# Kernel optimization log

Hardware: AMD Instinct MI355X
Metric: run time of the kernel (lower is better)

Reference implementation:

```python
import jax, jax.numpy as jnp
import numpy as np

DIM = 192
HEADS = 6
HEAD_DIM = DIM // HEADS
WS = (7, 7, 7)
SHIFT = (3, 3, 3)
RES = (14, 56, 56)
MLP_HIDDEN = DIM * 4
N = WS[0] * WS[1] * WS[2]  # 343 tokens per window
SCALE = HEAD_DIM ** (-0.5)


def _rel_pos_index():
    coords = np.stack(np.meshgrid(np.arange(WS[0]), np.arange(WS[1]), np.arange(WS[2]), indexing='ij'))
    cf = coords.reshape(3, -1)  # (3, N)
    rel = (cf[:, :, None] - cf[:, None, :]).transpose(1, 2, 0).astype(np.int64)  # (N, N, 3)
    rel[..., 0] += WS[0] - 1
    rel[..., 1] += WS[1] - 1
    rel[..., 2] += WS[2] - 1
    rel[..., 0] *= (2 * WS[1] - 1) * (2 * WS[2] - 1)
    rel[..., 1] *= 2 * WS[2] - 1
    return rel.sum(-1)  # (N, N)


def _attn_mask():
    S, H, W = RES
    img = np.zeros((S, H, W), dtype=np.float32)
    cnt = 0
    for s in (slice(0, -WS[0]), slice(-WS[0], -SHIFT[0]), slice(-SHIFT[0], None)):
        for h in (slice(0, -WS[1]), slice(-WS[1], -SHIFT[1]), slice(-SHIFT[1], None)):
            for w in (slice(0, -WS[2]), slice(-WS[2], -SHIFT[2]), slice(-SHIFT[2], None)):
                img[s, h, w] = cnt
                cnt += 1
    m = img.reshape(S // WS[0], WS[0], H // WS[1], WS[1], W // WS[2], WS[2])
    m = m.transpose(0, 2, 4, 1, 3, 5).reshape(-1, N)  # (nW, N)
    diff = m[:, None, :] - m[:, :, None]
    return np.where(diff != 0, -100.0, 0.0).astype(np.float32)  # (nW, N, N)


REL_IDX = jnp.asarray(_rel_pos_index())
ATTN_MASK = jnp.asarray(_attn_mask())


def _window_partition(x):
    # x: (B, S, H, W, C) -> (B*nW, N, C)
    B, S, H, W, C = x.shape
    x = x.reshape(B, S // WS[0], WS[0], H // WS[1], WS[1], W // WS[2], WS[2], C)
    x = x.transpose(0, 1, 3, 5, 2, 4, 6, 7)
    return x.reshape(-1, N, C)


def _window_reverse(wins, B):
    S, H, W = RES
    C = wins.shape[-1]
    x = wins.reshape(B, S // WS[0], H // WS[1], W // WS[2], WS[0], WS[1], WS[2], C)
    x = x.transpose(0, 1, 4, 2, 5, 3, 6, 7)
    return x.reshape(B, S, H, W, C)


def _layernorm(x, g, b):
    mu = x.mean(-1, keepdims=True)
    var = ((x - mu) ** 2).mean(-1, keepdims=True)
    return (x - mu) * jax.lax.rsqrt(var + 1e-5) * g + b


def setup_inputs() -> dict:
    key = jax.random.key(0)
    ks = jax.random.split(key, 16)
    p = lambda k, shape, s=0.02: (jax.random.normal(k, shape, dtype=jnp.float32) * s)
    return {
        'x': jax.random.normal(ks[0], (1, DIM) + RES, dtype=jnp.float32),
        'norm1_g': jnp.ones((DIM,), jnp.float32),
        'norm1_b': jnp.zeros((DIM,), jnp.float32),
        'qkv_w': p(ks[1], (DIM, 3 * DIM)),
        'qkv_b': jnp.zeros((3 * DIM,), jnp.float32),
        'rpb_table': p(ks[2], ((2 * WS[0] - 1) * (2 * WS[1] - 1) * (2 * WS[2] - 1), HEADS)),
        'proj_w': p(ks[3], (DIM, DIM)),
        'proj_b': jnp.zeros((DIM,), jnp.float32),
        'norm2_g': jnp.ones((DIM,), jnp.float32),
        'norm2_b': jnp.zeros((DIM,), jnp.float32),
        'fc1_w': p(ks[4], (DIM, MLP_HIDDEN)),
        'fc1_b': jnp.zeros((MLP_HIDDEN,), jnp.float32),
        'fc2_w': p(ks[5], (MLP_HIDDEN, DIM)),
        'fc2_b': jnp.zeros((DIM,), jnp.float32),
    }


def reference(x, norm1_g, norm1_b, qkv_w, qkv_b, rpb_table, proj_w, proj_b,
              norm2_g, norm2_b, fc1_w, fc1_b, fc2_w, fc2_b):
    B, C, S, H, W = x.shape
    L = S * H * W
    xt = x.transpose(0, 2, 3, 4, 1).reshape(B, L, C)  # b (s h w) c
    shortcut = xt
    xn = _layernorm(xt, norm1_g, norm1_b).reshape(B, S, H, W, C)
    xs = jnp.roll(xn, (-SHIFT[0], -SHIFT[1], -SHIFT[2]), axis=(1, 2, 3))
    xw = _window_partition(xs)  # (B*nW, N, C)
    B_ = xw.shape[0]
    nW = B_ // B

    qkv = (xw @ qkv_w + qkv_b).reshape(B_, N, 3, HEADS, HEAD_DIM)
    q = qkv[:, :, 0].transpose(0, 2, 1, 3) * SCALE  # (B_, h, N, d)
    k = qkv[:, :, 1].transpose(0, 2, 1, 3)
    v = qkv[:, :, 2].transpose(0, 2, 1, 3)

    attn = jnp.einsum('bhnd,bhmd->bhnm', q, k)
    bias = rpb_table[REL_IDX.reshape(-1)].reshape(N, N, HEADS).transpose(2, 0, 1)  # (h, N, N)
    attn = attn + bias[None]
    attn = attn.reshape(B, nW, HEADS, N, N) + ATTN_MASK[None, :, None]
    attn = jax.nn.softmax(attn.reshape(B_, HEADS, N, N), axis=-1)

    out = jnp.einsum('bhnm,bhmd->bhnd', attn, v).transpose(0, 2, 1, 3).reshape(B_, N, C)
    out = out @ proj_w + proj_b

    xr = _window_reverse(out, B)
    xr = jnp.roll(xr, (SHIFT[0], SHIFT[1], SHIFT[2]), axis=(1, 2, 3)).reshape(B, L, C)
    xt = shortcut + xr

    h = _layernorm(xt, norm2_g, norm2_b)
    h = jax.nn.gelu(h @ fc1_w + fc1_b, approximate=False) @ fc2_w + fc2_b
    xt = xt + h

    return xt.reshape(B, S, H, W, C).transpose(0, 4, 1, 2, 3)  # (B, C, S, H, W)
```

## Files before the change

kernel.cpp:

```cpp
#include <hip/hip_runtime.h>
#include <hip/hip_bf16.h>
#include <math.h>

#define L_TOK 43904
#define NWIN 128
#define NTOK 343
#define NHEAD 6
#define SCALE 0.17677669529663687f
#define LOG2E 1.4426950408889634f
#define NMASK -144.26950408889634f
#define BSTRIDE 352

typedef __attribute__((ext_vector_type(8))) short short8;
typedef __attribute__((ext_vector_type(4))) float f32x4;

__device__ __forceinline__ unsigned short f2bf(float x) {
    union { float f; unsigned int u; } v; v.f = x;
    unsigned int r = v.u + 0x7fffu + ((v.u >> 16) & 1u);
    return (unsigned short)(r >> 16);
}
__device__ __forceinline__ unsigned int pk2(float a, float b) {
    return (unsigned int)f2bf(a) | ((unsigned int)f2bf(b) << 16);
}
__device__ __forceinline__ void gload16(const void* g, void* l) {
    __builtin_amdgcn_global_load_lds((const __attribute__((address_space(1))) void*)g,
                                     (__attribute__((address_space(3))) void*)l, 16, 0, 0);
}

__device__ __forceinline__ int winrow(int l) {
    int s = l / 3136;
    int rem = l - s * 3136;
    int h = rem / 56;
    int w = rem - h * 56;
    int ps = s + 11; if (ps >= 14) ps -= 14;
    int ph = h + 53; if (ph >= 56) ph -= 56;
    int pw = w + 53; if (pw >= 56) pw -= 56;
    int wi = ((ps / 7) * 8 + ph / 7) * 8 + pw / 7;
    int tk = ((ps % 7) * 7 + ph % 7) * 7 + pw % 7;
    return wi * NTOK + tk;
}

__global__ __launch_bounds__(256) void convert_weights(
    const float* __restrict__ qkv_w, const float* __restrict__ qkv_b,
    const float* __restrict__ proj_w, const float* __restrict__ fc1_w,
    const float* __restrict__ fc2_w,
    unsigned short* __restrict__ qkvT, unsigned short* __restrict__ projT,
    unsigned short* __restrict__ fc1T, unsigned short* __restrict__ fc2T,
    float* __restrict__ qkvb_s) {
    int stride = gridDim.x * 256;
    int t0 = blockIdx.x * 256 + threadIdx.x;
    const float qs = SCALE * LOG2E;
    for (int i = t0; i < 576 * 192; i += stride) {
        int n = i / 192, k = i - n * 192;
        float v = qkv_w[k * 576 + n];
        if (n < 192) v *= qs;
        qkvT[i] = f2bf(v);
    }
    for (int i = t0; i < 192 * 192; i += stride) {
        int n = i / 192, k = i - n * 192;
        projT[i] = f2bf(proj_w[k * 192 + n]);
    }
    for (int i = t0; i < 768 * 192; i += stride) {
        int n = i / 192, k = i - n * 192;
        fc1T[i] = f2bf(fc1_w[k * 768 + n]);
    }
    for (int i = t0; i < 192 * 768; i += stride) {
        int n = i / 768, k = i - n * 768;
        fc2T[i] = f2bf(fc2_w[k * 192 + n]);
    }
    for (int i = t0; i < 576; i += stride) {
        float v = qkv_b[i]; if (i < 192) v *= qs;
        qkvb_s[i] = v;
    }
}

__global__ __launch_bounds__(256) void bias_compact(const float* __restrict__ table, float* __restrict__ biasC) {
    int q = blockIdx.x;
    int qs = q / 49, qh = (q / 7) % 7, qw = q % 7;
    for (int k = threadIdx.x; k < BSTRIDE; k += 256) {
        if (k < NTOK) {
            int ks = k / 49, kh = (k / 7) % 7, kw = k % 7;
            int idx = ((qs - ks + 6) * 13 + (qh - kh + 6)) * 13 + (qw - kw + 6);
            #pragma unroll
            for (int h = 0; h < NHEAD; ++h)
                biasC[((size_t)h * NTOK + q) * BSTRIDE + k] = table[idx * 6 + h] * LOG2E;
        } else {
            #pragma unroll
            for (int h = 0; h < NHEAD; ++h)
                biasC[((size_t)h * NTOK + q) * BSTRIDE + k] = -30000.f;
        }
    }
}

__global__ __launch_bounds__(256) void ln1_part(const float* __restrict__ x,
                                                const float* __restrict__ g, const float* __restrict__ b,
                                                float* __restrict__ xt, unsigned short* __restrict__ xw) {
    __shared__ float tile[192 * 65];
    __shared__ float red[4][64];
    __shared__ float red2[4][64];
    __shared__ float mu_s[64], rs_s[64];
    int l0 = blockIdx.x * 64;
    int tid = threadIdx.x;
    int j = tid & 63, c4 = tid >> 6;
    for (int cb = 0; cb < 192; cb += 4)
        tile[(cb + c4) * 65 + j] = x[(size_t)(cb + c4) * L_TOK + l0 + j];
    __syncthreads();
    float s = 0.f, ss = 0.f;
    for (int c = c4 * 48; c < c4 * 48 + 48; ++c) {
        float v = tile[c * 65 + j];
        s += v; ss += v * v;
    }
    red[c4][j] = s; red2[c4][j] = ss;
    __syncthreads();
    if (tid < 64) {
        float S = red[0][j] + red[1][j] + red[2][j] + red[3][j];
        float SS = red2[0][j] + red2[1][j] + red2[2][j] + red2[3][j];
        float mu = S * (1.f / 192.f);
        float var = SS * (1.f / 192.f) - mu * mu;
        mu_s[j] = mu;
        rs_s[j] = rsqrtf(var + 1e-5f);
    }
    __syncthreads();
    int wave = tid >> 6, lid = tid & 63;
    for (int t = wave; t < 64; t += 4) {
        int l = l0 + t;
        int r = winrow(l);
        float mu = mu_s[t], rs = rs_s[t];
        #pragma unroll
        for (int q = 0; q < 3; ++q) {
            int c = q * 64 + lid;
            float v = tile[c * 65 + t];
            xt[(size_t)l * 192 + c] = v;
            xw[(size_t)r * 192 + c] = f2bf((v - mu) * rs * g[c] + b[c]);
        }
    }
}

template<int EPI, int OUTMODE>
__global__ __launch_bounds__(256, 3) void gemm_bf16(
    const unsigned short* __restrict__ A, const unsigned short* __restrict__ Bt,
    const float* __restrict__ bias, void* __restrict__ Cout,
    const float* __restrict__ xt, int N, int K) {
    __shared__ unsigned char smem[49152];
    unsigned short* sh = (unsigned short*)smem;
    const int tid = threadIdx.x;
    const int m0 = blockIdx.x * 128;
    const int n0 = blockIdx.y * 64;
    const int lane = tid & 63, wv = tid >> 6;
    const int wm = wv >> 1, wn = wv & 1;
    const int lr = lane & 15, lg = lane >> 4;
    const int KT = K >> 6;

    f32x4 acc[4][2];
    #pragma unroll
    for (int i = 0; i < 4; ++i)
        #pragma unroll
        for (int jj = 0; jj < 2; ++jj)
            acc[i][jj] = (f32x4){0.f, 0.f, 0.f, 0.f};

    #define STAGE(BUF, K0) { \
        unsigned short* dst = sh + (BUF) * 12288; \
        _Pragma("unroll") \
        for (int i_ = 0; i_ < 4; ++i_) { \
            int g_ = (i_ * 4 + wv) * 64 + lane; \
            int row_ = g_ >> 3, gc_ = g_ & 7; \
            gload16(A + (size_t)(m0 + row_) * K + (K0) + ((gc_ ^ (row_ & 7)) << 3), dst + g_ * 8); \
        } \
        _Pragma("unroll") \
        for (int i_ = 0; i_ < 2; ++i_) { \
            int g_ = (i_ * 4 + wv) * 64 + lane; \
            int row_ = g_ >> 3, gc_ = g_ & 7; \
            gload16(Bt + (size_t)(n0 + row_) * K + (K0) + ((gc_ ^ (row_ & 7)) << 3), dst + 8192 + g_ * 8); \
        } }

    STAGE(0, 0);
    __syncthreads();
    for (int kt = 0; kt < KT; ++kt) {
        int buf = kt & 1;
        if (kt + 1 < KT) STAGE(buf ^ 1, (kt + 1) << 6);
        const unsigned short* sA = sh + buf * 12288;
        const unsigned short* sB = sA + 8192;
        #pragma unroll
        for (int kk = 0; kk < 2; ++kk) {
            short8 a[4], b[2];
            #pragma unroll
            for (int i = 0; i < 4; ++i) {
                int row = wm * 64 + i * 16 + lr;
                a[i] = *(const short8*)(sA + row * 64 + (((kk * 4 + lg) ^ (lr & 7)) << 3));
            }
            #pragma unroll
            for (int jj = 0; jj < 2; ++jj) {
                int row = wn * 32 + jj * 16 + lr;
                b[jj] = *(const short8*)(sB + row * 64 + (((kk * 4 + lg) ^ (lr & 7)) << 3));
            }
            #pragma unroll
            for (int i = 0; i < 4; ++i)
                #pragma unroll
                for (int jj = 0; jj < 2; ++jj)
                    acc[i][jj] = __builtin_amdgcn_mfma_f32_16x16x32_bf16(a[i], b[jj], acc[i][jj], 0, 0, 0);
        }
        __syncthreads();
    }
    #undef STAGE

    if (OUTMODE == 2) {
        float* Cs = (float*)smem;
        #pragma unroll
        for (int i = 0; i < 4; ++i)
            #pragma unroll
            for (int jj = 0; jj < 2; ++jj)
                #pragma unroll
                for (int r = 0; r < 4; ++r) {
                    int row = wm * 64 + i * 16 + lg * 4 + r;
                    int col = wn * 32 + jj * 16 + lr;
                    float v = acc[i][jj][r] + bias[n0 + col] + xt[(size_t)(m0 + row) * 192 + n0 + col];
                    Cs[row * 68 + col] = v;
                }
        __syncthreads();
        float* outp = (float*)Cout;
        int c = tid & 63;
        #pragma unroll
        for (int j4 = tid >> 6; j4 < 32; j4 += 4) {
            f32x4 v;
            #pragma unroll
            for (int t = 0; t < 4; ++t) v[t] = Cs[(j4 * 4 + t) * 68 + c];
            *(f32x4*)&outp[(size_t)(n0 + c) * L_TOK + m0 + j4 * 4] = v;
        }
    } else {
        float bia[2];
        bia[0] = bias[n0 + wn * 32 + lr];
        bia[1] = bias[n0 + wn * 32 + 16 + lr];
        #pragma unroll
        for (int i = 0; i < 4; ++i) {
            #pragma unroll
            for (int jj = 0; jj < 2; ++jj) {
                #pragma unroll
                for (int r = 0; r < 4; ++r) {
                    float v = acc[i][jj][r] + bia[jj];
                    if (EPI == 1) v = 0.5f * v * (1.f + erff(v * 0.70710678118654752f));
                    int row = m0 + wm * 64 + i * 16 + lg * 4 + r;
                    int col = n0 + wn * 32 + jj * 16 + lr;
                    if (OUTMODE == 1) ((float*)Cout)[(size_t)row * N + col] = v;
                    else ((unsigned short*)Cout)[(size_t)row * N + col] = f2bf(v);
                }
            }
        }
    }
}

__global__ __launch_bounds__(256) void attn_flash(
    const unsigned short* __restrict__ qkv, const float* __restrict__ biasC,
    unsigned short* __restrict__ aout) {
    __shared__ unsigned short Ks[352 * 32];
    __shared__ unsigned short Vt[32][360];
    __shared__ unsigned int Ps2[4][16][20];
    __shared__ unsigned char regq[352];
    const int w = blockIdx.x, h = blockIdx.y;
    const int tid = threadIdx.x;
    const size_t base = (size_t)w * NTOK * 576;

    for (int g = tid; g < 1372; g += 256)
        gload16(qkv + base + (size_t)(g >> 2) * 576 + 192 + h * 32 + ((g & 3) << 3), Ks + g * 8);
    if (tid < 36) {
        short8 z = {};
        *(short8*)(Ks + (343 + (tid >> 2)) * 32 + (tid & 3) * 8) = z;
    }
    for (int idx = tid; idx < 688; idx += 256) {
        int jp = idx >> 2, c = idx & 3;
        int j0 = jp * 2, j1 = j0 + 1;
        short8 v0 = *(const short8*)(qkv + base + (size_t)j0 * 576 + 384 + h * 32 + c * 8);
        short8 v1 = {};
        if (j1 < NTOK) v1 = *(const short8*)(qkv + base + (size_t)j1 * 576 + 384 + h * 32 + c * 8);
        #pragma unroll
        for (int i = 0; i < 8; ++i) {
            ushort2 pr; pr.x = (unsigned short)v0[i]; pr.y = (unsigned short)v1[i];
            *(ushort2*)&Vt[c * 8 + i][j0] = pr;
        }
    }
    for (int idx = tid; idx < 128; idx += 256) {
        ushort2 z; z.x = 0; z.y = 0;
        *(ushort2*)&Vt[idx >> 2][344 + (idx & 3) * 2] = z;
    }
    {
        const int wis = w >> 6, wih = (w >> 3) & 7, wiw = w & 7;
        for (int n = tid; n < 352; n += 256) {
            unsigned char rv = 0;
            if (n < NTOK) {
                int ts = n / 49, r49 = n - ts * 49, th = r49 / 7, tw = r49 - th * 7;
                int ps = wis * 7 + ts, ph = wih * 7 + th, pw = wiw * 7 + tw;
                int rs = ps < 7 ? 0 : (ps < 11 ? 1 : 2);
                int rh = ph < 49 ? 0 : (ph < 53 ? 1 : 2);
                int rw = pw < 49 ? 0 : (pw < 53 ? 1 : 2);
                rv = (unsigned char)(rs * 9 + rh * 3 + rw);
            }
            regq[n] = rv;
        }
    }
    __syncthreads();

    const int wid = tid >> 6, l = tid & 63, lr = l & 15, lg = l >> 4;

    for (int qt = wid; qt < 22; qt += 4) {
        int qrow = qt * 16 + lr;
        int qr = qrow < NTOK ? qrow : NTOK - 1;
        short8 qa = *(const short8*)(qkv + base + (size_t)qr * 576 + h * 32 + lg * 8);
        unsigned int rq = regq[qr];
        const float* bq = biasC + ((size_t)h * NTOK + qr) * BSTRIDE + lg * 4;

        float m_run = -1e30f, lsum = 0.f;
        f32x4 o0 = (f32x4){0.f, 0.f, 0.f, 0.f};
        f32x4 o1 = (f32x4){0.f, 0.f, 0.f, 0.f};
        const f32x4 zv = (f32x4){0.f, 0.f, 0.f, 0.f};

        f32x4 bv0 = *(const f32x4*)(bq);
        f32x4 bv1 = *(const f32x4*)(bq + 16);

        #pragma unroll 1
        for (int kb = 0; kb < 11; ++kb) {
            const int kt0 = 2 * kb, kt1 = 2 * kb + 1;
            short8 k0 = *(const short8*)(Ks + (kt0 * 16 + lr) * 32 + lg * 8);
            short8 k1 = *(const short8*)(Ks + (kt1 * 16 + lr) * 32 + lg * 8);
            f32x4 s0 = __builtin_amdgcn_mfma_f32_16x16x32_bf16(k0, qa, zv, 0, 0, 0);
            f32x4 s1 = __builtin_amdgcn_mfma_f32_16x16x32_bf16(k1, qa, zv, 0, 0, 0);
            f32x4 nb0 = zv, nb1 = zv;
            if (kb < 10) {
                nb0 = *(const f32x4*)(bq + (kt0 + 2) * 16);
                nb1 = *(const f32x4*)(bq + (kt1 + 2) * 16);
            }
            unsigned int rb0 = *(const unsigned int*)&regq[kt0 * 16 + lg * 4];
            unsigned int rb1 = *(const unsigned int*)&regq[kt1 * 16 + lg * 4];
            #pragma unroll
            for (int r = 0; r < 4; ++r) {
                s0[r] += bv0[r] + ((((rb0 >> (r * 8)) & 255u) != rq) ? NMASK : 0.f);
                s1[r] += bv1[r] + ((((rb1 >> (r * 8)) & 255u) != rq) ? NMASK : 0.f);
            }
            float tm = fmaxf(fmaxf(fmaxf(s0[0], s0[1]), fmaxf(s0[2], s0[3])),
                             fmaxf(fmaxf(s1[0], s1[1]), fmaxf(s1[2], s1[3])));
            tm = fmaxf(tm, __shfl_xor(tm, 16));
            tm = fmaxf(tm, __shfl_xor(tm, 32));
            float m_new = fmaxf(m_run, tm);
            float alpha = exp2f(m_run - m_new);
            m_run = m_new;
            lsum *= alpha;
            #pragma unroll
            for (int r = 0; r < 4; ++r) { o0[r] *= alpha; o1[r] *= alpha; }
            f32x4 p0, p1;
            #pragma unroll
            for (int r = 0; r < 4; ++r) {
                p0[r] = exp2f(s0[r] - m_run);
                p1[r] = exp2f(s1[r] - m_run);
                lsum += p0[r] + p1[r];
            }
            Ps2[wid][lr][lg * 2 + 0] = pk2(p0[0], p0[1]);
            Ps2[wid][lr][lg * 2 + 1] = pk2(p0[2], p0[3]);
            Ps2[wid][lr][8 + lg * 2 + 0] = pk2(p1[0], p1[1]);
            Ps2[wid][lr][8 + lg * 2 + 1] = pk2(p1[2], p1[3]);
            short8 pa = *(const short8*)&Ps2[wid][lr][lg * 4];
            short8 v0 = *(const short8*)&Vt[lr][kb * 32 + lg * 8];
            short8 v1 = *(const short8*)&Vt[16 + lr][kb * 32 + lg * 8];
            o0 = __builtin_amdgcn_mfma_f32_16x16x32_bf16(pa, v0, o0, 0, 0, 0);
            o1 = __builtin_amdgcn_mfma_f32_16x16x32_bf16(pa, v1, o1, 0, 0, 0);
            bv0 = nb0; bv1 = nb1;
        }
        lsum += __shfl_xor(lsum, 16);
        lsum += __shfl_xor(lsum, 32);
        float inv = 1.f / lsum;

        #pragma unroll
        for (int r = 0; r < 4; ++r) {
            float iv = __shfl(inv, lg * 4 + r);
            int q = qt * 16 + lg * 4 + r;
            if (q < NTOK) {
                size_t orow = ((size_t)w * NTOK + q) * 192 + h * 32;
                aout[orow + lr] = f2bf(o0[r] * iv);
                aout[orow + 16 + lr] = f2bf(o1[r] * iv);
            }
        }
    }
}

__global__ __launch_bounds__(256) void add_res_ln2(float* __restrict__ xt, const float* __restrict__ pout,
                                                   const float* __restrict__ g, const float* __restrict__ b,
                                                   unsigned short* __restrict__ h1) {
    int l0 = blockIdx.x * 64;
    int wave = threadIdx.x >> 6, lid = threadIdx.x & 63;
    for (int t = wave; t < 64; t += 4) {
        int l = l0 + t;
        int r = winrow(l);
        float v[3];
        float s = 0.f, ss = 0.f;
        #pragma unroll
        for (int q = 0; q < 3; ++q) {
            int c = q * 64 + lid;
            float val = xt[(size_t)l * 192 + c] + pout[(size_t)r * 192 + c];
            xt[(size_t)l * 192 + c] = val;
            v[q] = val;
            s += val; ss += val * val;
        }
        #pragma unroll
        for (int off = 32; off; off >>= 1) {
            s += __shfl_xor(s, off);
            ss += __shfl_xor(ss, off);
        }
        float mu = s * (1.f / 192.f);
        float rs = rsqrtf(ss * (1.f / 192.f) - mu * mu + 1e-5f);
        #pragma unroll
        for (int q = 0; q < 3; ++q) {
            int c = q * 64 + lid;
            h1[(size_t)l * 192 + c] = f2bf((v[q] - mu) * rs * g[c] + b[c]);
        }
    }
}

extern "C" void kernel_launch(void* const* d_in, const int* in_sizes, int n_in,
                              void* d_out, int out_size, void* d_ws, size_t ws_size,
                              hipStream_t stream) {
    const float* x      = (const float*)d_in[0];
    const float* n1g    = (const float*)d_in[1];
    const float* n1b    = (const float*)d_in[2];
    const float* qkv_w  = (const float*)d_in[3];
    const float* qkv_b  = (const float*)d_in[4];
    const float* rpb    = (const float*)d_in[5];
    const float* proj_w = (const float*)d_in[6];
    const float* proj_b = (const float*)d_in[7];
    const float* n2g    = (const float*)d_in[8];
    const float* n2b    = (const float*)d_in[9];
    const float* fc1_w  = (const float*)d_in[10];
    const float* fc1_b  = (const float*)d_in[11];
    const float* fc2_w  = (const float*)d_in[12];
    const float* fc2_b  = (const float*)d_in[13];
    float* out = (float*)d_out;

    char* p = (char*)d_ws;
    float* xt = (float*)p;                     p += (size_t)L_TOK * 192 * 4;
    float* pout = (float*)p;                   p += (size_t)L_TOK * 192 * 4;
    unsigned short* xw = (unsigned short*)p;
    unsigned short* h1 = xw;                   p += (size_t)L_TOK * 192 * 2;
    unsigned short* qkvb = (unsigned short*)p;
    unsigned short* h2 = qkvb;                 p += (size_t)L_TOK * 768 * 2;
    unsigned short* aoutb = (unsigned short*)p; p += (size_t)L_TOK * 192 * 2;
    float* biasC = (float*)p;                  p += (size_t)NHEAD * NTOK * BSTRIDE * 4 + 256;
    unsigned short* qkvT = (unsigned short*)p; p += (size_t)576 * 192 * 2;
    unsigned short* projT = (unsigned short*)p; p += (size_t)192 * 192 * 2;
    unsigned short* fc1T = (unsigned short*)p; p += (size_t)768 * 192 * 2;
    unsigned short* fc2T = (unsigned short*)p; p += (size_t)192 * 768 * 2;
    float* qkvb_s = (float*)p;                 p += 576 * 4;

    convert_weights<<<576, 256, 0, stream>>>(qkv_w, qkv_b, proj_w, fc1_w, fc2_w,
                                             qkvT, projT, fc1T, fc2T, qkvb_s);
    bias_compact<<<343, 256, 0, stream>>>(rpb, biasC);
    ln1_part<<<686, 256, 0, stream>>>(x, n1g, n1b, xt, xw);
    gemm_bf16<0, 0><<<dim3(343, 9), 256, 0, stream>>>(xw, qkvT, qkvb_s, qkvb, nullptr, 576, 192);
    attn_flash<<<dim3(NWIN, NHEAD), 256, 0, stream>>>(qkvb, biasC, aoutb);
    gemm_bf16<0, 1><<<dim3(343, 3), 256, 0, stream>>>(aoutb, projT, proj_b, pout, nullptr, 192, 192);
    add_res_ln2<<<686, 256, 0, stream>>>(xt, pout, n2g, n2b, h1);
    gemm_bf16<1, 0><<<dim3(343, 12), 256, 0, stream>>>(h1, fc1T, fc1_b, h2, nullptr, 768, 192);
    gemm_bf16<0, 2><<<dim3(343, 3), 256, 0, stream>>>(h2, fc2T, fc2_b, out, xt, 192, 768);
}
```

Measured before the change: 271.8 us.

## Fuse projection GEMM with residual add and LayerNorm2; swizzle K tile in attention

Replaces the projection GEMM plus the separate add-residual/LayerNorm kernel with one kernel. Each block computes 64 rows across all 192 output columns, then adds the bias and residual, scatters the rows back through the window-reverse and roll mapping, and writes both xt and the normalized bf16 h1. This removes the fp32 pout round trip and one launch. In exchange it uses fewer, larger blocks, holds 12 accumulators per wave, and writes scattered rows. The attention kernel also XOR-swizzles K chunks in shared memory to reduce LDS bank conflicts.

Result: faster. 259.1 us (-4.7%).

```diff
diff --git a/kernel.cpp b/kernel.cpp
--- a/kernel.cpp
+++ b/kernel.cpp
@@ -248,6 +248,90 @@
     }
 }
 
+__global__ __launch_bounds__(256) void gemm_proj_ln(
+    const unsigned short* __restrict__ A, const unsigned short* __restrict__ Bt,
+    const float* __restrict__ bias, const float* __restrict__ g2, const float* __restrict__ b2,
+    float* __restrict__ xt, unsigned short* __restrict__ h1) {
+    __shared__ unsigned short As[2][64 * 64];
+    __shared__ unsigned short Bs[2][192 * 64];
+    const int tid = threadIdx.x;
+    const int m0 = blockIdx.x * 64;
+    const int lane = tid & 63, wv = tid >> 6;
+    const int lr = lane & 15, lg = lane >> 4;
+    const int K = 192;
+
+    f32x4 acc[12];
+    #pragma unroll
+    for (int jj = 0; jj < 12; ++jj) acc[jj] = (f32x4){0.f, 0.f, 0.f, 0.f};
+
+    #define PSTAGE(BUF, K0) { \
+        _Pragma("unroll") \
+        for (int i_ = 0; i_ < 2; ++i_) { \
+            int g_ = i_ * 256 + tid; \
+            int row_ = g_ >> 3, gc_ = g_ & 7; \
+            gload16(A + (size_t)(m0 + row_) * K + (K0) + ((gc_ ^ (row_ & 7)) << 3), &As[BUF][g_ * 8]); \
+        } \
+        _Pragma("unroll") \
+        for (int i_ = 0; i_ < 6; ++i_) { \
+            int g_ = i_ * 256 + tid; \
+            int row_ = g_ >> 3, gc_ = g_ & 7; \
+            gload16(Bt + (size_t)row_ * K + (K0) + ((gc_ ^ (row_ & 7)) << 3), &Bs[BUF][g_ * 8]); \
+        } }
+
+    PSTAGE(0, 0);
+    __syncthreads();
+    for (int kt = 0; kt < 3; ++kt) {
+        int buf = kt & 1;
+        if (kt + 1 < 3) PSTAGE(buf ^ 1, (kt + 1) << 6);
+        #pragma unroll
+        for (int kk = 0; kk < 2; ++kk) {
+            int arow = wv * 16 + lr;
+            short8 a = *(const short8*)(&As[buf][arow * 64 + (((kk * 4 + lg) ^ (lr & 7)) << 3)]);
+            #pragma unroll
+            for (int jj = 0; jj < 12; ++jj) {
+                int brow = jj * 16 + lr;
+                short8 b = *(const short8*)(&Bs[buf][brow * 64 + (((kk * 4 + lg) ^ (lr & 7)) << 3)]);
+                acc[jj] = __builtin_amdgcn_mfma_f32_16x16x32_bf16(a, b, acc[jj], 0, 0, 0);
+            }
+        }
+        __syncthreads();
+    }
+    #undef PSTAGE
+
+    #pragma unroll
+    for (int r = 0; r < 4; ++r) {
+        int m = m0 + wv * 16 + lg * 4 + r;
+        int wi = m / 343, tk = m - wi * 343;
+        int ts = tk / 49, rm = tk - ts * 49, th = rm / 7, tw = rm - th * 7;
+        int ps = (wi >> 6) * 7 + ts, ph = ((wi >> 3) & 7) * 7 + th, pw = (wi & 7) * 7 + tw;
+        int ss_ = ps + 3; if (ss_ >= 14) ss_ -= 14;
+        int hh = ph + 3; if (hh >= 56) hh -= 56;
+        int ww = pw + 3; if (ww >= 56) ww -= 56;
+        size_t l = ((size_t)ss_ * 56 + hh) * 56 + ww;
+        float val[12];
+        float sum = 0.f, ssum = 0.f;
+        #pragma unroll
+        for (int jj = 0; jj < 12; ++jj) {
+            int col = jj * 16 + lr;
+            float v = acc[jj][r] + bias[col] + xt[l * 192 + col];
+            xt[l * 192 + col] = v;
+            val[jj] = v; sum += v; ssum += v * v;
+        }
+        #pragma unroll
+        for (int off = 1; off < 16; off <<= 1) {
+            sum += __shfl_xor(sum, off);
+            ssum += __shfl_xor(ssum, off);
+        }
+        float mu = sum * (1.f / 192.f);
+        float rs = rsqrtf(ssum * (1.f / 192.f) - mu * mu + 1e-5f);
+        #pragma unroll
+        for (int jj = 0; jj < 12; ++jj) {
+            int col = jj * 16 + lr;
+            h1[l * 192 + col] = f2bf((val[jj] - mu) * rs * g2[col] + b2[col]);
+        }
+    }
+}
+
 __global__ __launch_bounds__(256) void attn_flash(
     const unsigned short* __restrict__ qkv, const float* __restrict__ biasC,
     unsigned short* __restrict__ aout) {
@@ -259,8 +343,10 @@
     const int tid = threadIdx.x;
     const size_t base = (size_t)w * NTOK * 576;
 
-    for (int g = tid; g < 1372; g += 256)
-        gload16(qkv + base + (size_t)(g >> 2) * 576 + 192 + h * 32 + ((g & 3) << 3), Ks + g * 8);
+    for (int g = tid; g < 1372; g += 256) {
+        int row = g >> 2, c = g & 3;
+        gload16(qkv + base + (size_t)row * 576 + 192 + h * 32 + ((c ^ ((row >> 1) & 3)) << 3), Ks + g * 8);
+    }
     if (tid < 36) {
         short8 z = {};
         *(short8*)(Ks + (343 + (tid >> 2)) * 32 + (tid & 3) * 8) = z;
@@ -299,6 +385,7 @@
     __syncthreads();
 
     const int wid = tid >> 6, l = tid & 63, lr = l & 15, lg = l >> 4;
+    const int kchunk = (lg ^ ((lr >> 1) & 3)) << 3;
 
     for (int qt = wid; qt < 22; qt += 4) {
         int qrow = qt * 16 + lr;
@@ -318,8 +405,8 @@
         #pragma unroll 1
         for (int kb = 0; kb < 11; ++kb) {
             const int kt0 = 2 * kb, kt1 = 2 * kb + 1;
-            short8 k0 = *(const short8*)(Ks + (kt0 * 16 + lr) * 32 + lg * 8);
-            short8 k1 = *(const short8*)(Ks + (kt1 * 16 + lr) * 32 + lg * 8);
+            short8 k0 = *(const short8*)(Ks + (kt0 * 16 + lr) * 32 + kchunk);
+            short8 k1 = *(const short8*)(Ks + (kt1 * 16 + lr) * 32 + kchunk);
             f32x4 s0 = __builtin_amdgcn_mfma_f32_16x16x32_bf16(k0, qa, zv, 0, 0, 0);
             f32x4 s1 = __builtin_amdgcn_mfma_f32_16x16x32_bf16(k1, qa, zv, 0, 0, 0);
             f32x4 nb0 = zv, nb1 = zv;
@@ -375,39 +462,6 @@
                 aout[orow + lr] = f2bf(o0[r] * iv);
                 aout[orow + 16 + lr] = f2bf(o1[r] * iv);
             }
-        }
-    }
-}
-
-__global__ __launch_bounds__(256) void add_res_ln2(float* __restrict__ xt, const float* __restrict__ pout,
-                                                   const float* __restrict__ g, const float* __restrict__ b,
-                                                   unsigned short* __restrict__ h1) {
-    int l0 = blockIdx.x * 64;
-    int wave = threadIdx.x >> 6, lid = threadIdx.x & 63;
-    for (int t = wave; t < 64; t += 4) {
-        int l = l0 + t;
-        int r = winrow(l);
-        float v[3];
-        float s = 0.f, ss = 0.f;
-        #pragma unroll
-        for (int q = 0; q < 3; ++q) {
-            int c = q * 64 + lid;
-            float val = xt[(size_t)l * 192 + c] + pout[(size_t)r * 192 + c];
-            xt[(size_t)l * 192 + c] = val;
-            v[q] = val;
-            s += val; ss += val * val;
-        }
-        #pragma unroll
-        for (int off = 32; off; off >>= 1) {
-            s += __shfl_xor(s, off);
-            ss += __shfl_xor(ss, off);
-        }
-        float mu = s * (1.f / 192.f);
-        float rs = rsqrtf(ss * (1.f / 192.f) - mu * mu + 1e-5f);
-        #pragma unroll
-        for (int q = 0; q < 3; ++q) {
-            int c = q * 64 + lid;
-            h1[(size_t)l * 192 + c] = f2bf((v[q] - mu) * rs * g[c] + b[c]);
         }
     }
 }
@@ -433,7 +487,6 @@
 
     char* p = (char*)d_ws;
     float* xt = (float*)p;                     p += (size_t)L_TOK * 192 * 4;
-    float* pout = (float*)p;                   p += (size_t)L_TOK * 192 * 4;
     unsigned short* xw = (unsigned short*)p;
     unsigned short* h1 = xw;                   p += (size_t)L_TOK * 192 * 2;
     unsigned short* qkvb = (unsigned short*)p;
@@ -452,8 +505,7 @@
     ln1_part<<<686, 256, 0, stream>>>(x, n1g, n1b, xt, xw);
     gemm_bf16<0, 0><<<dim3(343, 9), 256, 0, stream>>>(xw, qkvT, qkvb_s, qkvb, nullptr, 576, 192);
     attn_flash<<<dim3(NWIN, NHEAD), 256, 0, stream>>>(qkvb, biasC, aoutb);
-    gemm_bf16<0, 1><<<dim3(343, 3), 256, 0, stream>>>(aoutb, projT, proj_b, pout, nullptr, 192, 192);
-    add_res_ln2<<<686, 256, 0, stream>>>(xt, pout, n2g, n2b, h1);
+    gemm_proj_ln<<<686, 256, 0, stream>>>(aoutb, projT, proj_b, n2g, n2b, xt, h1);
     gemm_bf16<1, 0><<<dim3(343, 12), 256, 0, stream>>>(h1, fc1T, fc1_b, h2, nullptr, 768, 192);
     gemm_bf16<0, 2><<<dim3(343, 3), 256, 0, stream>>>(h2, fc2T, fc2_b, out, xt, 192, 768);
 }
```
